# Optimization experiments

Measured on AMD Instinct MI355X. Metric: run time of the kernel, lower is better.

The kernel has to match this reference:

```python
import jax, jax.numpy as jnp
import numpy as np

B, SEQ, PRED, ENC = 32, 720, 96, 321
LAYERS, SCALE = 2, 2
SEG = [48, 24]
D = [512, 256]
SNX = [SEQ // s for s in SEG]   # [15, 30]
SNY = [PRED // s for s in SEG]  # [2, 4]


def _gru(x, h, Wih, Whh, bih, bhh):
    # torch.nn.GRUCell math
    gi = x @ Wih.T + bih
    gh = h @ Whh.T + bhh
    i_r, i_z, i_n = jnp.split(gi, 3, axis=-1)
    h_r, h_z, h_n = jnp.split(gh, 3, axis=-1)
    r = jax.nn.sigmoid(i_r + h_r)
    z = jax.nn.sigmoid(i_z + h_z)
    n = jnp.tanh(i_n + r * h_n)
    return (1.0 - z) * n + z * h


def setup_inputs():
    key = jax.random.key(0)
    ks = iter(jax.random.split(key, 40))
    inp = {"x": jax.random.normal(next(ks), (B, SEQ, ENC), jnp.float32)}
    sc = 0.02
    for i in range(LAYERS):
        d, s = D[i], SEG[i]
        inp[f"W_emb{i}"] = jax.random.normal(next(ks), (d, s), jnp.float32) * sc
        inp[f"b_emb{i}"] = jnp.zeros((d,), jnp.float32)
        inp[f"Wih{i}"] = jax.random.normal(next(ks), (3 * d, d), jnp.float32) * sc
        inp[f"Whh{i}"] = jax.random.normal(next(ks), (3 * d, d), jnp.float32) * sc
        inp[f"bih{i}"] = jnp.zeros((3 * d,), jnp.float32)
        inp[f"bhh{i}"] = jnp.zeros((3 * d,), jnp.float32)
        inp[f"Wpred{i}"] = jax.random.normal(next(ks), (s, d), jnp.float32) * sc
        inp[f"bpred{i}"] = jnp.zeros((s,), jnp.float32)
        inp[f"pos{i}"] = jax.random.normal(next(ks), (SNY[i], d // 2), jnp.float32)
        inp[f"chan{i}"] = jax.random.normal(next(ks), (ENC, d // 2), jnp.float32)
    return inp


def _forward(x, params):
    seq_last = jax.lax.stop_gradient(x[:, -1:, :])   # [B,1,ENC] (detached in torch)
    xc = (x - seq_last).transpose(0, 2, 1)            # [B,ENC,SEQ]
    out = jnp.zeros((B, PRED, ENC), x.dtype)
    for i in range(LAYERS):
        p = params[i]
        d, s, T, S = D[i], SEG[i], SNX[i], SNY[i]
        # value embedding: [B*ENC, T, seg_len] -> [B*ENC, T, d]
        xe = jax.nn.relu(jnp.einsum('nts,ds->ntd', xc.reshape(-1, T, s), p['W_emb']) + p['b_emb'])
        if i == 0:
            seq = xe.transpose(1, 0, 2)   # all seg_num_x[0] segments in order
        else:
            # faithful to source: finer layer always consumes segments 0..scale^(i+1)-1
            # once per outer step, seg_num_x[0] times in total
            k = SCALE ** (i + 1)
            idx = np.tile(np.arange(k), SNX[0])
            seq = xe[:, idx].transpose(1, 0, 2)
        h0 = jnp.zeros((xe.shape[0], d), x.dtype)
        step = lambda h, xt: (_gru(xt, h, p['Wih'], p['Whh'], p['bih'], p['bhh']), None)
        h_fin, _ = jax.lax.scan(step, h0, seq)   # [B*ENC, d]
        # decoder: seg_num_y independent GRU cell applications (no carried state)
        half = d // 2
        pos = jnp.concatenate([
            jnp.broadcast_to(p['pos'][None], (ENC, S, half)),
            jnp.broadcast_to(p['chan'][:, None], (ENC, S, half))], axis=-1).reshape(ENC * S, d)
        pos = jnp.tile(pos, (B, 1)).reshape(S, B * ENC, d)   # contiguous chunks per step
        hn = jnp.repeat(h_fin, S, axis=0).reshape(S, B * ENC, d)
        hy = _gru(pos, hn, p['Wih'], p['Whh'], p['bih'], p['bhh'])   # [S, B*ENC, d]
        y = hy.reshape(S * B * ENC, d) @ p['Wpred'].T + p['bpred']   # [S*B*ENC, seg_len]
        y = y.reshape(-1, ENC, PRED).transpose(0, 2, 1)              # [B, PRED, ENC]
        out = out + y + seq_last
    return out / LAYERS


def reference(x, W_emb0, b_emb0, Wih0, Whh0, bih0, bhh0, Wpred0, bpred0, pos0, chan0,
              W_emb1, b_emb1, Wih1, Whh1, bih1, bhh1, Wpred1, bpred1, pos1, chan1):
    params = [
        dict(W_emb=W_emb0, b_emb=b_emb0, Wih=Wih0, Whh=Whh0, bih=bih0, bhh=bhh0,
             Wpred=Wpred0, bpred=bpred0, pos=pos0, chan=chan0),
        dict(W_emb=W_emb1, b_emb=b_emb1, Wih=Wih1, Whh=Whh1, bih=bih1, bhh=bhh1,
             Wpred=Wpred1, bpred=bpred1, pos=pos1, chan=chan1),
    ]
    return _forward(x, params)
```

## Files before the change

kernel.cpp:

```cpp
#include <hip/hip_runtime.h>
#include <math.h>


#define NB     10272
#define MP     10368
#define ENC_   321
#define SEQ_   720
#define PRED_  96
#define BATCH_ 32

typedef long long i64;
typedef unsigned short u16;
typedef unsigned int u32;
using bf16x8 = __attribute__((ext_vector_type(8))) short;
using f32x4  = __attribute__((ext_vector_type(4))) float;

#define AS1 __attribute__((address_space(1)))
#define AS3 __attribute__((address_space(3)))
#define GLOAD16(g, l) __builtin_amdgcn_global_load_lds((const AS1 void*)(g), (AS3 void*)(l), 16, 0, 0)

__device__ __forceinline__ float bf2f(u16 u) {
    union { u32 i; float f; } v; v.i = ((u32)u) << 16; return v.f;
}
__device__ __forceinline__ u16 f2bf(float f) {
    union { float f; u32 i; } v; v.f = f;
    return (u16)((v.i + 0x7fff + ((v.i >> 16) & 1)) >> 16);
}
__device__ __forceinline__ float sigf(float x) {
    x = fminf(fmaxf(x, -30.f), 30.f);
    return 1.f / (1.f + __expf(-x));
}
__device__ __forceinline__ float tanhfast(float x) {
    x = fminf(fmaxf(x, -15.f), 15.f);
    float e = __expf(2.f * x);
    return (e - 1.f) / (e + 1.f);
}
__device__ __forceinline__ float bsel(uint2 u, int r) {
    u32 wv = (r & 2) ? u.y : u.x;
    return bf2f((u16)((r & 1) ? (wv >> 16) : (wv & 0xffff)));
}
__device__ __forceinline__ void swz(int idx, int NXT, int NYT, int& mt, int& nt) {
    int per = NYT * 8;
    int grp = idx / per;
    int base = grp * 8;
    int mg = NXT - base; if (mg > 8) mg = 8;
    int rem = idx - grp * per;
    mt = base + rem % mg;
    nt = rem / mg;
}

__global__ __launch_bounds__(256) void zero2_kernel(float* __restrict__ a,
                                                    u16* __restrict__ b, i64 n) {
    i64 i = (i64)blockIdx.x * 256 + threadIdx.x;
    if (i < n) { a[i] = 0.f; b[i] = 0; }
}

__global__ __launch_bounds__(256) void convert_pad(const float* __restrict__ src,
                                                   u16* __restrict__ dst,
                                                   int R, int C, int Rp, int Cp) {
    i64 idx = (i64)blockIdx.x * 256 + threadIdx.x;
    i64 total = (i64)Rp * Cp;
    if (idx >= total) return;
    int r = (int)(idx / Cp);
    int c = (int)(idx - (i64)r * Cp);
    dst[idx] = (r < R && c < C) ? f2bf(src[(i64)r * C + c]) : (u16)0;
}

__global__ __launch_bounds__(256) void seg_gather_bf(const float* __restrict__ x,
                                                     u16* __restrict__ dst,
                                                     int t0, int T, int s, int Kp) {
    i64 idx = (i64)blockIdx.x * 256 + threadIdx.x;
    i64 per_t = (i64)MP * Kp;
    i64 total = (i64)T * per_t;
    if (idx >= total) return;
    int t = (int)(idx / per_t);
    i64 rem = idx - (i64)t * per_t;
    int j = (int)(rem / MP);
    int n = (int)(rem - (i64)j * MP);
    float v = 0.f;
    if (n < NB && j < s) {
        int b = n / ENC_, e = n - b * ENC_;
        const float* xb = x + (i64)b * SEQ_ * ENC_ + e;
        v = xb[(i64)((t0 + t) * s + j) * ENC_] - xb[(i64)(SEQ_ - 1) * ENC_];
    }
    dst[((i64)t * MP + n) * Kp + j] = f2bf(v);
}

__global__ __launch_bounds__(256) void pmat_fill_bf(const float* __restrict__ pos,
                                                    const float* __restrict__ chan,
                                                    u16* __restrict__ dst,
                                                    int S, int d, int Rp) {
    i64 idx = (i64)blockIdx.x * 256 + threadIdx.x;
    i64 total = (i64)Rp * d;
    if (idx >= total) return;
    int row = (int)(idx / d);
    int c = (int)(idx - (i64)row * d);
    float v = 0.f;
    if (row < ENC_ * S) {
        int e = row / S, sy = row - e * S;
        int half = d >> 1;
        v = (c < half) ? pos[sy * half + c] : chan[e * half + (c - half)];
    }
    dst[idx] = f2bf(v);
}

__global__ __launch_bounds__(256) void out_kernel(const float* __restrict__ x,
                                                  const float* __restrict__ y0,
                                                  const float* __restrict__ y1,
                                                  float* __restrict__ out) {
    int idx = blockIdx.x * 256 + threadIdx.x;
    const int total = BATCH_ * PRED_ * ENC_;
    if (idx >= total) return;
    int b = idx / (PRED_ * ENC_);
    int r = idx - b * (PRED_ * ENC_);
    int p = r / ENC_;
    int e = r - p * ENC_;
    int n = b * ENC_ + e;
    float sl = x[(i64)b * SEQ_ * ENC_ + (i64)(SEQ_ - 1) * ENC_ + e];
    out[idx] = sl + 0.5f * (y0[(i64)n * PRED_ + p] + y1[(i64)n * PRED_ + p]);
}

template<int MODE>
__global__ __launch_bounds__(256) void gemm_bf16mfma(const u16* __restrict__ A,
                                                     const u16* __restrict__ B,
                                                     const float* __restrict__ bias,
                                                     void* __restrict__ Cp,
                                                     int K, int Mstore, int Nstore,
                                                     int ldc, int NXT, int NYT) {
    __shared__ u16 smA[128 * 64];
    __shared__ u16 smB[128 * 64];
    const int tid = threadIdx.x;
    const int w = tid >> 6, l = tid & 63;
    int mt, nt; swz(blockIdx.x, NXT, NYT, mt, nt);
    const int m0 = mt * 128, n0 = nt * 128;
    const int srow = (l >> 3) & 7, pch = l & 7;
    const int cch = pch ^ srow;
    const u16* ga[4]; const u16* gb[4];
#pragma unroll
    for (int r = 0; r < 4; ++r) {
        int seg = r * 4 + w;
        ga[r] = A + (i64)(m0 + seg * 8 + srow) * K + cch * 8;
        gb[r] = B + (i64)(n0 + seg * 8 + srow) * K + cch * 8;
    }
    f32x4 acc[4][4] = {};
    const int lr = l & 15, lg = l >> 4;
    const int wm = (w >> 1) * 64, wn = (w & 1) * 64;
    for (int kk = 0; kk < K; kk += 64) {
#pragma unroll
        for (int r = 0; r < 4; ++r) { GLOAD16(ga[r], smA + (r * 4 + w) * 512); ga[r] += 64; }
#pragma unroll
        for (int r = 0; r < 4; ++r) { GLOAD16(gb[r], smB + (r * 4 + w) * 512); gb[r] += 64; }
        __syncthreads();
#pragma unroll
        for (int s = 0; s < 2; ++s) {
            const int ph = ((s * 4 + lg) ^ (lr & 7)) * 8;
            bf16x8 av[4], bv[4];
#pragma unroll
            for (int i = 0; i < 4; ++i)
                av[i] = *(const bf16x8*)(smA + (wm + i * 16 + lr) * 64 + ph);
#pragma unroll
            for (int j = 0; j < 4; ++j)
                bv[j] = *(const bf16x8*)(smB + (wn + j * 16 + lr) * 64 + ph);
#pragma unroll
            for (int i = 0; i < 4; ++i)
#pragma unroll
                for (int j = 0; j < 4; ++j)
                    acc[i][j] = __builtin_amdgcn_mfma_f32_16x16x32_bf16(av[i], bv[j], acc[i][j], 0, 0, 0);
        }
        __syncthreads();
    }
#pragma unroll
    for (int i = 0; i < 4; ++i) {
        int mbase = m0 + wm + i * 16 + 4 * lg;
#pragma unroll
        for (int j = 0; j < 4; ++j) {
            int c = n0 + wn + j * 16 + lr;
            if (c >= Nstore) continue;
            float bs = bias[c];
#pragma unroll
            for (int r = 0; r < 4; ++r) {
                int mm = mbase + r;
                if (mm < Mstore) {
                    float v = acc[i][j][r] + bs;
                    if (MODE == 2) v = fmaxf(v, 0.f);
                    if (MODE == 0) ((float*)Cp)[(i64)mm * ldc + c] = v;
                    else           ((u16*)Cp)[(i64)mm * ldc + c] = f2bf(v);
                }
            }
        }
    }
}

template<int D>
__global__ __launch_bounds__(256, 3) void gru_step(const u16* __restrict__ xe,
                                                   const u16* __restrict__ hsrc,
                                                   const u16* __restrict__ Wih,
                                                   const u16* __restrict__ Whh,
                                                   const float* __restrict__ bih,
                                                   const float* __restrict__ bhh,
                                                   f32x4* __restrict__ hfrag,
                                                   u16* __restrict__ hdst) {
    constexpr int NCT = D / 16;
    __shared__ u16 smA[64 * 64];
    __shared__ u16 smB[3 * 64 * 64];
    const int tid = threadIdx.x;
    const int w = tid >> 6, l = tid & 63;
    const int m0 = blockIdx.x * 64;
    const int c0 = blockIdx.y * 64;
    const int srow = (l >> 3) & 7, pch = l & 7;
    const int cch = pch ^ srow;
    const int lr = l & 15, lg = l >> 4;
    f32x4 aR[4] = {}, aZ[4] = {}, aNI[4] = {}, aNH[4] = {};
#pragma unroll
    for (int phase = 0; phase < 2; ++phase) {
        const u16* Abase = phase ? hsrc : xe;
        const u16* Bbase = phase ? Whh : Wih;
        const u16* ga[2]; const u16* gb[6];
#pragma unroll
        for (int r = 0; r < 2; ++r)
            ga[r] = Abase + (i64)(m0 + (r * 4 + w) * 8 + srow) * D + cch * 8;
#pragma unroll
        for (int q = 0; q < 6; ++q) {
            int gs = q * 4 + w;
            int g = gs >> 3, sp = gs & 7;
            gb[q] = Bbase + (i64)(g * D + c0 + sp * 8 + srow) * D + cch * 8;
        }
        for (int kk = 0; kk < D; kk += 64) {
#pragma unroll
            for (int r = 0; r < 2; ++r) { GLOAD16(ga[r], smA + (r * 4 + w) * 512); ga[r] += 64; }
#pragma unroll
            for (int q = 0; q < 6; ++q) { GLOAD16(gb[q], smB + (q * 4 + w) * 512); gb[q] += 64; }
            __syncthreads();
#pragma unroll
            for (int s = 0; s < 2; ++s) {
                const int phs = ((s * 4 + lg) ^ (lr & 7)) * 8;
                bf16x8 av = *(const bf16x8*)(smA + (w * 16 + lr) * 64 + phs);
#pragma unroll
                for (int j = 0; j < 4; ++j) {
                    bf16x8 b0 = *(const bf16x8*)(smB + 0 * 4096 + (j * 16 + lr) * 64 + phs);
                    bf16x8 b1 = *(const bf16x8*)(smB + 1 * 4096 + (j * 16 + lr) * 64 + phs);
                    bf16x8 b2 = *(const bf16x8*)(smB + 2 * 4096 + (j * 16 + lr) * 64 + phs);
                    aR[j] = __builtin_amdgcn_mfma_f32_16x16x32_bf16(av, b0, aR[j], 0, 0, 0);
                    aZ[j] = __builtin_amdgcn_mfma_f32_16x16x32_bf16(av, b1, aZ[j], 0, 0, 0);
                    if (phase == 0)
                        aNI[j] = __builtin_amdgcn_mfma_f32_16x16x32_bf16(av, b2, aNI[j], 0, 0, 0);
                    else
                        aNH[j] = __builtin_amdgcn_mfma_f32_16x16x32_bf16(av, b2, aNH[j], 0, 0, 0);
                }
            }
            __syncthreads();
        }
    }
    const int Trow = (m0 >> 4) + w;
    const int rowb = m0 + w * 16 + 4 * lg;
#pragma unroll
    for (int j = 0; j < 4; ++j) {
        const int cc = c0 + j * 16 + lr;
        const i64 tb = (i64)Trow * NCT + ((c0 >> 4) + j);
        f32x4 ho = hfrag[tb * 64 + l];
        float bR = bih[cc] + bhh[cc];
        float bZ = bih[D + cc] + bhh[D + cc];
        float bNI = bih[2 * D + cc];
        float bNH = bhh[2 * D + cc];
        f32x4 hn;
#pragma unroll
        for (int r = 0; r < 4; ++r) {
            float rr = sigf(aR[j][r] + bR);
            float zz = sigf(aZ[j][r] + bZ);
            float nn = tanhfast(aNI[j][r] + bNI + rr * (aNH[j][r] + bNH));
            hn[r] = (1.f - zz) * nn + zz * ho[r];
        }
        hfrag[tb * 64 + l] = hn;
#pragma unroll
        for (int r = 0; r < 4; ++r)
            hdst[(i64)(rowb + r) * D + cc] = f2bf(hn[r]);
    }
}

template<int D, int S>
__global__ __launch_bounds__(256) void gru_dec(const u16* __restrict__ Asrc,
                                               const u16* __restrict__ Whh,
                                               const float* __restrict__ bhh,
                                               const u16* __restrict__ gi,
                                               const f32x4* __restrict__ hfrag,
                                               u16* __restrict__ hy) {
    constexpr int NCT = D / 16;
    constexpr int NYT = D / 64;
    __shared__ u16 smA[128 * 64];
    __shared__ u16 smB[3 * 64 * 64];
    const int tid = threadIdx.x;
    const int w = tid >> 6, l = tid & 63;
    int mt, nt; swz(blockIdx.x, 81, NYT, mt, nt);
    const int m0 = mt * 128;
    const int c0 = nt * 64;
    const int srow = (l >> 3) & 7, pch = l & 7;
    const int cch = pch ^ srow;
    const u16* ga[4]; const u16* gb[6];
#pragma unroll
    for (int r = 0; r < 4; ++r)
        ga[r] = Asrc + (i64)(m0 + (r * 4 + w) * 8 + srow) * D + cch * 8;
#pragma unroll
    for (int q = 0; q < 6; ++q) {
        int gs = q * 4 + w;
        int g = gs >> 3, sp = gs & 7;
        gb[q] = Whh + (i64)(g * D + c0 + sp * 8 + srow) * D + cch * 8;
    }
    f32x4 acc[3][4][2] = {};
    const int lr = l & 15, lg = l >> 4;
    const int wm = (w >> 1) * 64, wc = (w & 1) * 32;
    for (int kk = 0; kk < D; kk += 64) {
#pragma unroll
        for (int r = 0; r < 4; ++r) { GLOAD16(ga[r], smA + (r * 4 + w) * 512); ga[r] += 64; }
#pragma unroll
        for (int q = 0; q < 6; ++q) { GLOAD16(gb[q], smB + (q * 4 + w) * 512); gb[q] += 64; }
        __syncthreads();
#pragma unroll
        for (int s = 0; s < 2; ++s) {
            const int ph = ((s * 4 + lg) ^ (lr & 7)) * 8;
            bf16x8 av[4], bv[3][2];
#pragma unroll
            for (int i = 0; i < 4; ++i)
                av[i] = *(const bf16x8*)(smA + (wm + i * 16 + lr) * 64 + ph);
#pragma unroll
            for (int g = 0; g < 3; ++g)
#pragma unroll
                for (int j = 0; j < 2; ++j)
                    bv[g][j] = *(const bf16x8*)(smB + g * 4096 + (wc + j * 16 + lr) * 64 + ph);
#pragma unroll
            for (int g = 0; g < 3; ++g)
#pragma unroll
                for (int i = 0; i < 4; ++i)
#pragma unroll
                    for (int j = 0; j < 2; ++j)
                        acc[g][i][j] = __builtin_amdgcn_mfma_f32_16x16x32_bf16(av[i], bv[g][j], acc[g][i][j], 0, 0, 0);
        }
        __syncthreads();
    }
#pragma unroll
    for (int i = 0; i < 4; ++i) {
        const int Trow = (m0 + wm + 16 * i) >> 4;
        const int rowb = m0 + wm + 16 * i + 4 * lg;
#pragma unroll
        for (int j = 0; j < 2; ++j) {
            const int cc = c0 + wc + 16 * j + lr;
            const int ct = (c0 + wc + 16 * j) >> 4;
            const i64 tb = (i64)Trow * NCT + ct;
            float b0 = bhh[cc], b1 = bhh[D + cc], b2 = bhh[2 * D + cc];
            f32x4 ho = hfrag[tb * 64 + l];
#pragma unroll
            for (int r = 0; r < 4; ++r) {
                int mm = rowb + r;
                if (mm >= NB) continue;
                int e = mm % ENC_;
                float hr = acc[0][i][j][r] + b0;
                float hz = acc[1][i][j][r] + b1;
                float hn2 = acc[2][i][j][r] + b2;
#pragma unroll
                for (int sy = 0; sy < S; ++sy) {
                    i64 gib = (i64)(e * S + sy) * 3 * D + cc;
                    float rr = sigf(bf2f(gi[gib]) + hr);
                    float zz = sigf(bf2f(gi[gib + D]) + hz);
                    float nn = tanhfast(bf2f(gi[gib + 2 * D]) + rr * hn2);
                    hy[((i64)mm * S + sy) * D + cc] = f2bf((1.f - zz) * nn + zz * ho[r]);
                }
            }
        }
    }
}

extern "C" void kernel_launch(void* const* d_in, const int* in_sizes, int n_in,
                              void* d_out, int out_size, void* d_ws, size_t ws_size,
                              hipStream_t stream) {
    const float* x      = (const float*)d_in[0];
    const float* W_emb0 = (const float*)d_in[1];
    const float* b_emb0 = (const float*)d_in[2];
    const float* Wih0   = (const float*)d_in[3];
    const float* Whh0   = (const float*)d_in[4];
    const float* bih0   = (const float*)d_in[5];
    const float* bhh0   = (const float*)d_in[6];
    const float* Wpred0 = (const float*)d_in[7];
    const float* bpred0 = (const float*)d_in[8];
    const float* pos0   = (const float*)d_in[9];
    const float* chan0  = (const float*)d_in[10];
    const float* W_emb1 = (const float*)d_in[11];
    const float* b_emb1 = (const float*)d_in[12];
    const float* Wih1   = (const float*)d_in[13];
    const float* Whh1   = (const float*)d_in[14];
    const float* bih1   = (const float*)d_in[15];
    const float* bhh1   = (const float*)d_in[16];
    const float* Wpred1 = (const float*)d_in[17];
    const float* bpred1 = (const float*)d_in[18];
    const float* pos1   = (const float*)d_in[19];
    const float* chan1  = (const float*)d_in[20];
    float* out = (float*)d_out;

    i64 off = 0;
    char* base = (char*)d_ws;
    auto alloc = [&](i64 bytes) -> void* {
        void* p = base + off; off += (bytes + 255) & ~(i64)255; return p;
    };
    float* f_hfrag = (float*)alloc((i64)MP * 512 * 4);
    u16*   f_mirA  = (u16*)  alloc((i64)MP * 512 * 2);
    u16*   f_mirB  = (u16*)  alloc((i64)MP * 512 * 2);
    u16*   wih0b   = (u16*)  alloc((i64)1536 * 512 * 2);
    u16*   whh0b   = (u16*)  alloc((i64)1536 * 512 * 2);
    u16*   wih1b   = (u16*)  alloc((i64)768 * 256 * 2);
    u16*   whh1b   = (u16*)  alloc((i64)768 * 256 * 2);
    u16*   we0b    = (u16*)  alloc((i64)512 * 64 * 2);
    u16*   we1b    = (u16*)  alloc((i64)256 * 64 * 2);
    u16*   wp0b    = (u16*)  alloc((i64)128 * 512 * 2);
    u16*   wp1b    = (u16*)  alloc((i64)128 * 256 * 2);
    u16*   f_pm0   = (u16*)  alloc((i64)768 * 512 * 2);
    u16*   f_pm1   = (u16*)  alloc((i64)1408 * 256 * 2);
    u16*   f_gidec = (u16*)  alloc((i64)768 * 1536 * 2);
    u16*   f_hy    = (u16*)  alloc((i64)4 * NB * 256 * 2);
    float* f_y0    = (float*)alloc((i64)NB * 96 * 4);
    float* f_y1    = (float*)alloc((i64)NB * 96 * 4);
    i64 fixed = off;

    char* R = base + fixed;
    i64 a1 = (((i64)4 * MP * 64 * 2) + 255) & ~(i64)255;
    i64 a2 = (i64)4 * MP * 256 * 2;
    i64 R1 = a1 + a2;
    u16* f_seg1 = (u16*)R;
    u16* f_xe1  = (u16*)(R + a1);
    int gsz = 1;
    {
        const int cand[4] = {15, 5, 3, 2};
        for (int ii = 0; ii < 4; ++ii) {
            i64 need = (i64)cand[ii] * MP * (64 + 512) * 2 + 2 * 256;
            i64 tot = fixed + (need > R1 ? need : R1);
            if (tot <= (i64)ws_size) { gsz = cand[ii]; break; }
        }
    }
    u16* f_seg0 = (u16*)R;
    i64 s1 = (((i64)gsz * MP * 64 * 2) + 255) & ~(i64)255;
    u16* f_xe0 = (u16*)(R + s1);

    auto cvt = [&](const float* s, u16* dst, int Rr, int C, int Rp, int Cp) {
        i64 tot = (i64)Rp * Cp;
        convert_pad<<<(int)((tot + 255) / 256), 256, 0, stream>>>(s, dst, Rr, C, Rp, Cp);
    };
    auto gemmN = [&](const u16* A, const u16* B, const float* bias, void* C,
                     int gx, int Nc, int K, int Mstore, int ldc, int mode) {
        int NYT = (Nc + 127) / 128;
        dim3 g(gx * NYT);
        if (mode == 0)      gemm_bf16mfma<0><<<g, 256, 0, stream>>>(A, B, bias, C, K, Mstore, Nc, ldc, gx, NYT);
        else if (mode == 1) gemm_bf16mfma<1><<<g, 256, 0, stream>>>(A, B, bias, C, K, Mstore, Nc, ldc, gx, NYT);
        else                gemm_bf16mfma<2><<<g, 256, 0, stream>>>(A, B, bias, C, K, Mstore, Nc, ldc, gx, NYT);
    };

    cvt(Wih0, wih0b, 1536, 512, 1536, 512);
    cvt(Whh0, whh0b, 1536, 512, 1536, 512);
    cvt(Wih1, wih1b, 768, 256, 768, 256);
    cvt(Whh1, whh1b, 768, 256, 768, 256);
    cvt(W_emb0, we0b, 512, 48, 512, 64);
    cvt(W_emb1, we1b, 256, 24, 256, 64);
    cvt(Wpred0, wp0b, 48, 512, 128, 512);
    cvt(Wpred1, wp1b, 24, 256, 128, 256);
    pmat_fill_bf<<<(int)(((i64)768 * 512 + 255) / 256), 256, 0, stream>>>(pos0, chan0, f_pm0, 2, 512, 768);
    pmat_fill_bf<<<(int)(((i64)1408 * 256 + 255) / 256), 256, 0, stream>>>(pos1, chan1, f_pm1, 4, 256, 1408);

    {
        i64 n = (i64)MP * 512;
        zero2_kernel<<<(int)((n + 255) / 256), 256, 0, stream>>>(f_hfrag, f_mirA, n);
    }
    for (int t0 = 0; t0 < 15;) {
        int g = 15 - t0 < gsz ? 15 - t0 : gsz;
        i64 tot = (i64)g * MP * 64;
        seg_gather_bf<<<(int)((tot + 255) / 256), 256, 0, stream>>>(x, f_seg0, t0, g, 48, 64);
        gemmN(f_seg0, we0b, b_emb0, f_xe0, g * 81, 512, 64, g * MP, 512, 2);
        for (int s = 0; s < g; ++s) {
            int tg = t0 + s;
            const u16* Asrc = (tg & 1) ? f_mirB : f_mirA;
            u16* Adst = (tg & 1) ? f_mirA : f_mirB;
            gru_step<512><<<dim3(162, 8), 256, 0, stream>>>(
                f_xe0 + (i64)s * MP * 512, Asrc, wih0b, whh0b, bih0, bhh0,
                (f32x4*)f_hfrag, Adst);
        }
        t0 += g;
    }
    gemmN(f_pm0, wih0b, bih0, f_gidec, 6, 1536, 512, 642, 1536, 1);
    gru_dec<512, 2><<<dim3(81 * 8), 256, 0, stream>>>(
        f_mirB, whh0b, bhh0, f_gidec, (const f32x4*)f_hfrag, f_hy);
    gemmN(f_hy, wp0b, bpred0, f_y0, 161, 48, 512, 2 * NB, 48, 0);

    {
        i64 n = (i64)MP * 256;
        zero2_kernel<<<(int)((n + 255) / 256), 256, 0, stream>>>(f_hfrag, f_mirA, n);
    }
    {
        i64 tot = (i64)4 * MP * 64;
        seg_gather_bf<<<(int)((tot + 255) / 256), 256, 0, stream>>>(x, f_seg1, 0, 4, 24, 64);
    }
    gemmN(f_seg1, we1b, b_emb1, f_xe1, 324, 256, 64, 4 * MP, 256, 2);
    for (int t = 0; t < 60; ++t) {
        const u16* Asrc = (t & 1) ? f_mirB : f_mirA;
        u16* Adst = (t & 1) ? f_mirA : f_mirB;
        gru_step<256><<<dim3(162, 4), 256, 0, stream>>>(
            f_xe1 + (i64)(t & 3) * MP * 256, Asrc, wih1b, whh1b, bih1, bhh1,
            (f32x4*)f_hfrag, Adst);
    }
    gemmN(f_pm1, wih1b, bih1, f_gidec, 11, 768, 256, 1284, 768, 1);
    gru_dec<256, 4><<<dim3(81 * 4), 256, 0, stream>>>(
        f_mirA, whh1b, bhh1, f_gidec, (const f32x4*)f_hfrag, f_hy);
    gemmN(f_hy, wp1b, bpred1, f_y1, 321, 24, 256, 4 * NB, 24, 0);

    out_kernel<<<(BATCH_ * PRED_ * ENC_ + 255) / 256, 256, 0, stream>>>(x, f_y0, f_y1, out);
}
```

Before: 2.427 ms.

## Precompute layer-1 input gate projections once instead of every recurrent step

Layer 1's recurrence cycles through only four distinct input segments over its 60 steps, so x·Wih is now computed once for those four with a single GEMM into a bf16 buffer. A new step kernel then does only the h·Whh product and reads the precomputed gates in its epilogue. This removes about half the MFMA work per step. In exchange it adds workspace, one upfront GEMM, uncoalesced bf16 gate reads in the epilogue, and bf16 rounding of the input gates.

```diff
diff --git a/kernel.cpp b/kernel.cpp
--- a/kernel.cpp
+++ b/kernel.cpp
@@ -34,10 +34,6 @@
     x = fminf(fmaxf(x, -15.f), 15.f);
     float e = __expf(2.f * x);
     return (e - 1.f) / (e + 1.f);
-}
-__device__ __forceinline__ float bsel(uint2 u, int r) {
-    u32 wv = (r & 2) ? u.y : u.x;
-    return bf2f((u16)((r & 1) ? (wv >> 16) : (wv & 0xffff)));
 }
 __device__ __forceinline__ void swz(int idx, int NXT, int NYT, int& mt, int& nt) {
     int per = NYT * 8;
@@ -268,6 +264,82 @@
             float rr = sigf(aR[j][r] + bR);
             float zz = sigf(aZ[j][r] + bZ);
             float nn = tanhfast(aNI[j][r] + bNI + rr * (aNH[j][r] + bNH));
+            hn[r] = (1.f - zz) * nn + zz * ho[r];
+        }
+        hfrag[tb * 64 + l] = hn;
+#pragma unroll
+        for (int r = 0; r < 4; ++r)
+            hdst[(i64)(rowb + r) * D + cc] = f2bf(hn[r]);
+    }
+}
+
+template<int D>
+__global__ __launch_bounds__(256, 3) void gru_step_h(const u16* __restrict__ gi,
+                                                     const u16* __restrict__ hsrc,
+                                                     const u16* __restrict__ Whh,
+                                                     const float* __restrict__ bhh,
+                                                     f32x4* __restrict__ hfrag,
+                                                     u16* __restrict__ hdst) {
+    constexpr int NCT = D / 16;
+    __shared__ u16 smA[64 * 64];
+    __shared__ u16 smB[3 * 64 * 64];
+    const int tid = threadIdx.x;
+    const int w = tid >> 6, l = tid & 63;
+    const int m0 = blockIdx.x * 64;
+    const int c0 = blockIdx.y * 64;
+    const int srow = (l >> 3) & 7, pch = l & 7;
+    const int cch = pch ^ srow;
+    const int lr = l & 15, lg = l >> 4;
+    f32x4 aR[4] = {}, aZ[4] = {}, aNH[4] = {};
+    const u16* ga[2]; const u16* gb[6];
+#pragma unroll
+    for (int r = 0; r < 2; ++r)
+        ga[r] = hsrc + (i64)(m0 + (r * 4 + w) * 8 + srow) * D + cch * 8;
+#pragma unroll
+    for (int q = 0; q < 6; ++q) {
+        int gs = q * 4 + w;
+        int g = gs >> 3, sp = gs & 7;
+        gb[q] = Whh + (i64)(g * D + c0 + sp * 8 + srow) * D + cch * 8;
+    }
+    for (int kk = 0; kk < D; kk += 64) {
+#pragma unroll
+        for (int r = 0; r < 2; ++r) { GLOAD16(ga[r], smA + (r * 4 + w) * 512); ga[r] += 64; }
+#pragma unroll
+        for (int q = 0; q < 6; ++q) { GLOAD16(gb[q], smB + (q * 4 + w) * 512); gb[q] += 64; }
+        __syncthreads();
+#pragma unroll
+        for (int s = 0; s < 2; ++s) {
+            const int phs = ((s * 4 + lg) ^ (lr & 7)) * 8;
+            bf16x8 av = *(const bf16x8*)(smA + (w * 16 + lr) * 64 + phs);
+#pragma unroll
+            for (int j = 0; j < 4; ++j) {
+                bf16x8 b0 = *(const bf16x8*)(smB + 0 * 4096 + (j * 16 + lr) * 64 + phs);
+                bf16x8 b1 = *(const bf16x8*)(smB + 1 * 4096 + (j * 16 + lr) * 64 + phs);
+                bf16x8 b2 = *(const bf16x8*)(smB + 2 * 4096 + (j * 16 + lr) * 64 + phs);
+                aR[j] = __builtin_amdgcn_mfma_f32_16x16x32_bf16(av, b0, aR[j], 0, 0, 0);
+                aZ[j] = __builtin_amdgcn_mfma_f32_16x16x32_bf16(av, b1, aZ[j], 0, 0, 0);
+                aNH[j] = __builtin_amdgcn_mfma_f32_16x16x32_bf16(av, b2, aNH[j], 0, 0, 0);
+            }
+        }
+        __syncthreads();
+    }
+    const int Trow = (m0 >> 4) + w;
+    const int rowb = m0 + w * 16 + 4 * lg;
+#pragma unroll
+    for (int j = 0; j < 4; ++j) {
+        const int cc = c0 + j * 16 + lr;
+        const i64 tb = (i64)Trow * NCT + ((c0 >> 4) + j);
+        f32x4 ho = hfrag[tb * 64 + l];
+        float bR = bhh[cc];
+        float bZ = bhh[D + cc];
+        float bNH = bhh[2 * D + cc];
+        f32x4 hn;
+#pragma unroll
+        for (int r = 0; r < 4; ++r) {
+            const u16* gp = gi + (i64)(rowb + r) * 3 * D + cc;
+            float rr = sigf(bf2f(gp[0]) + aR[j][r] + bR);
+            float zz = sigf(bf2f(gp[D]) + aZ[j][r] + bZ);
+            float nn = tanhfast(bf2f(gp[2 * D]) + rr * (aNH[j][r] + bNH));
             hn[r] = (1.f - zz) * nn + zz * ho[r];
         }
         hfrag[tb * 64 + l] = hn;
@@ -420,10 +492,12 @@
 
     char* R = base + fixed;
     i64 a1 = (((i64)4 * MP * 64 * 2) + 255) & ~(i64)255;
-    i64 a2 = (i64)4 * MP * 256 * 2;
-    i64 R1 = a1 + a2;
+    i64 a2 = (((i64)4 * MP * 256 * 2) + 255) & ~(i64)255;
+    i64 a3 = (i64)4 * MP * 768 * 2;
+    i64 R1 = a1 + a2 + a3;
     u16* f_seg1 = (u16*)R;
     u16* f_xe1  = (u16*)(R + a1);
+    u16* f_gi1  = (u16*)(R + a1 + a2);
     int gsz = 1;
     {
         const int cand[4] = {15, 5, 3, 2};
@@ -494,11 +568,12 @@
         seg_gather_bf<<<(int)((tot + 255) / 256), 256, 0, stream>>>(x, f_seg1, 0, 4, 24, 64);
     }
     gemmN(f_seg1, we1b, b_emb1, f_xe1, 324, 256, 64, 4 * MP, 256, 2);
+    gemmN(f_xe1, wih1b, bih1, f_gi1, 324, 768, 256, 4 * MP, 768, 1);
     for (int t = 0; t < 60; ++t) {
         const u16* Asrc = (t & 1) ? f_mirB : f_mirA;
         u16* Adst = (t & 1) ? f_mirA : f_mirB;
-        gru_step<256><<<dim3(162, 4), 256, 0, stream>>>(
-            f_xe1 + (i64)(t & 3) * MP * 256, Asrc, wih1b, whh1b, bih1, bhh1,
+        gru_step_h<256><<<dim3(162, 4), 256, 0, stream>>>(
+            f_gi1 + (i64)(t & 3) * MP * 768, Asrc, whh1b, bhh1,
             (f32x4*)f_hfrag, Adst);
     }
     gemmN(f_pm1, wih1b, bih1, f_gidec, 11, 768, 256, 1284, 768, 1);
```

After: 2.373 ms. 2.2% less time.
